# Optimization experiments

Hardware: AMD Instinct MI355X
Metric: run time of the kernel (lower is better)

Reference implementation:

```python
import jax, jax.numpy as jnp
import numpy as np
from jax import lax

DIM = 128
HEADS = 8
GROUPS = 8
DIM_HEAD = 64
DOWN = 4
OFF_SCALE = 4.0
KSIZE = 6
B, N, M = 2, 1024, 1024


def ln(x, g, b, eps=1e-5):
    m = x.mean(-1, keepdims=True)
    v = ((x - m) ** 2).mean(-1, keepdims=True)
    return (x - m) / jnp.sqrt(v + eps) * g + b


def grid_sample_1d(feats, grid):
    # feats: (Bg, C, Mk), grid: (Bg, Nd) normalized coords in [-1, 1]
    # bilinear, padding_mode='zeros', align_corners=False (torch semantics)
    Bg, C, Mk = feats.shape
    x = ((grid + 1.0) * Mk - 1.0) / 2.0
    x0 = jnp.floor(x)
    w1 = x - x0

    def gather(xi):
        valid = ((xi >= 0) & (xi <= Mk - 1)).astype(feats.dtype)
        idx = jnp.clip(xi, 0, Mk - 1).astype(jnp.int32)
        vals = jnp.take_along_axis(
            feats, jnp.broadcast_to(idx[:, None, :], (Bg, C, idx.shape[-1])), axis=2)
        return vals * valid[:, None, :]

    return gather(x0) * (1.0 - w1)[:, None, :] + gather(x0 + 1.0) * w1[:, None, :]


def deform_cross_attn(xq, xkv, qw, kw, vw, ow, ob, o1w, o1b, o2w,
                      c1w, c1b, c2w, c2b, c3w, c3b):
    # xq, xkv: (B, C, N) channel-first token streams
    Bb, C, Nq = xq.shape
    cg = C // GROUPS  # 16 channels per offset group
    q = jnp.einsum('bgcn,goc->bgon', xq.reshape(Bb, GROUPS, cg, Nq), qw)  # (B,g,64,N)
    gq = q.reshape(Bb * GROUPS, DIM_HEAD, Nq)
    pad = (KSIZE - DOWN) // 2
    off = lax.conv_general_dilated(gq, o1w[:, None, :], (DOWN,), [(pad, pad)],
                                   feature_group_count=DIM_HEAD,
                                   dimension_numbers=('NCH', 'OIH', 'NCH')) + o1b[None, :, None]
    off = jax.nn.gelu(off, approximate=False)
    off = jnp.tanh(jnp.einsum('bcn,c->bn', off, o2w)) * OFF_SCALE  # (B*g, Nd)
    Nd = off.shape[-1]
    vgrid = jnp.arange(Nd, dtype=off.dtype)[None] + off
    vgs = 2.0 * vgrid / max(Nd - 1, 1) - 1.0  # normalized sample positions
    xkv_g = xkv.reshape(Bb, GROUPS, cg, xkv.shape[-1]).reshape(Bb * GROUPS, cg, xkv.shape[-1])
    kv = grid_sample_1d(xkv_g, vgs).reshape(Bb, GROUPS, cg, Nd)
    k = jnp.einsum('bgcn,goc->bgon', kv, kw)
    v = jnp.einsum('bgcn,goc->bgon', kv, vw)
    sim = jnp.einsum('bhdi,bhdj->bhij', q * (DIM_HEAD ** -0.5), k)  # heads == groups
    seq = 2.0 * jnp.arange(Nq, dtype=vgs.dtype) / max(Nq - 1, 1) - 1.0
    rel = seq[None, :, None] - vgs[:, None, :]  # (B*g, N, Nd)
    bias = jnp.sign(rel) * jnp.log1p(jnp.abs(rel))
    h = jax.nn.relu(bias[..., None] * c1w[0] + c1b)  # CPB MLP, hidden=dim//4=32
    h = jax.nn.relu(h @ c2w + c2b)
    h = (h @ c3w + c3b)[..., 0]
    sim = sim + h.reshape(Bb, GROUPS, Nq, Nd)  # heads // offset_groups == 1
    attn = jax.nn.softmax(sim, axis=-1)
    out = jnp.einsum('bhij,bhdj->bhdi', attn, v).reshape(Bb, GROUPS * DIM_HEAD, Nq)
    out = jnp.einsum('bcn,oc->bon', out, ow) + ob[:, None]
    return out, attn


def mha(q_in, kv_in, w_in, b_in, w_out, b_out):
    # seq-first torch nn.MultiheadAttention, eval mode (no dropout)
    E = DIM; h = HEADS; dh = E // h
    q = q_in @ w_in[:E].T + b_in[:E]
    k = kv_in @ w_in[E:2 * E].T + b_in[E:2 * E]
    v = kv_in @ w_in[2 * E:].T + b_in[2 * E:]
    Lq, Bb, _ = q.shape
    Lk = k.shape[0]
    qh = q.reshape(Lq, Bb, h, dh).transpose(1, 2, 0, 3)
    kh = k.reshape(Lk, Bb, h, dh).transpose(1, 2, 0, 3)
    vh = v.reshape(Lk, Bb, h, dh).transpose(1, 2, 0, 3)
    attn = jax.nn.softmax(jnp.einsum('bhid,bhjd->bhij', qh, kh) * (dh ** -0.5), axis=-1)
    out = jnp.einsum('bhij,bhjd->bhid', attn, vh).transpose(2, 0, 1, 3).reshape(Lq, Bb, E)
    return out @ w_out.T + b_out


def transfusion(x1, x2, ng, nb, inw, inb, ow, ob, pw, pb):
    x = x1 + mha(ln(x1, ng, nb), ln(x2, ng, nb), inw, inb, ow, ob)
    x = ln(x.transpose(1, 0, 2), ng, nb)  # (B, N, E)
    return jnp.tanh(x.mean(1) @ pw.T + pb)[:, None, :]  # (B, 1, E)


def setup_inputs():
    key = jax.random.key(0)
    ks = iter(jax.random.split(key, 40))
    rn = lambda shape, s=0.05: jax.random.normal(next(ks), shape, dtype=jnp.float32) * s
    return {
        'x1_0': rn((B, N, DIM), 1.0),
        'x1_1': rn((B, N, DIM), 1.0),
        'x2': rn((B, M, DIM), 1.0),
        'norm_g': jnp.ones((DIM,), jnp.float32),
        'norm_b': jnp.zeros((DIM,), jnp.float32),
        'd_qw': rn((2, GROUPS, DIM_HEAD, DIM // GROUPS)),
        'd_kw': rn((2, GROUPS, DIM_HEAD, DIM // GROUPS)),
        'd_vw': rn((2, GROUPS, DIM_HEAD, DIM // GROUPS)),
        'd_ow': rn((2, DIM, GROUPS * DIM_HEAD)),
        'd_ob': jnp.zeros((2, DIM), jnp.float32),
        'd_off1w': rn((2, DIM_HEAD, KSIZE)),
        'd_off1b': jnp.zeros((2, DIM_HEAD), jnp.float32),
        'd_off2w': rn((2, DIM_HEAD)),
        'd_cpb_w1': rn((2, 1, 32)),
        'd_cpb_b1': jnp.zeros((2, 32), jnp.float32),
        'd_cpb_w2': rn((2, 32, 32)),
        'd_cpb_b2': jnp.zeros((2, 32), jnp.float32),
        'd_cpb_w3': rn((2, 32, 1)),
        'd_cpb_b3': jnp.zeros((2, 1), jnp.float32),
        'fus_w': rn((DIM, 2 * DIM)),
        'fus_b': jnp.zeros((DIM,), jnp.float32),
        'tf_ng': jnp.ones((2, DIM), jnp.float32),
        'tf_nb': jnp.zeros((2, DIM), jnp.float32),
        'tf_inw': rn((2, 3 * DIM, DIM)),
        'tf_inb': jnp.zeros((2, 3 * DIM), jnp.float32),
        'tf_ow': rn((2, DIM, DIM)),
        'tf_ob': jnp.zeros((2, DIM), jnp.float32),
        'tf_pw': rn((2, DIM, DIM)),
        'tf_pb': jnp.zeros((2, DIM), jnp.float32),
        'attn_dim': 128,
    }


def reference(x1_0, x1_1, x2, norm_g, norm_b, d_qw, d_kw, d_vw, d_ow, d_ob,
              d_off1w, d_off1b, d_off2w, d_cpb_w1, d_cpb_b1, d_cpb_w2, d_cpb_b2,
              d_cpb_w3, d_cpb_b3, fus_w, fus_b, tf_ng, tf_nb, tf_inw, tf_inb,
              tf_ow, tf_ob, tf_pw, tf_pb, attn_dim):
    nkv = ln(x2, norm_g, norm_b).transpose(0, 2, 1)
    xo1, a1 = deform_cross_attn(ln(x1_0, norm_g, norm_b).transpose(0, 2, 1), nkv,
                                d_qw[0], d_kw[0], d_vw[0], d_ow[0], d_ob[0],
                                d_off1w[0], d_off1b[0], d_off2w[0],
                                d_cpb_w1[0], d_cpb_b1[0], d_cpb_w2[0], d_cpb_b2[0],
                                d_cpb_w3[0], d_cpb_b3[0])
    xo2, a2 = deform_cross_attn(ln(x1_1, norm_g, norm_b).transpose(0, 2, 1), nkv,
                                d_qw[1], d_kw[1], d_vw[1], d_ow[1], d_ob[1],
                                d_off1w[1], d_off1b[1], d_off2w[1],
                                d_cpb_w1[1], d_cpb_b1[1], d_cpb_w2[1], d_cpb_b2[1],
                                d_cpb_w3[1], d_cpb_b3[1])
    xout1 = x1_0 + xo1.transpose(0, 2, 1)
    xout2 = x1_1 + xo2.transpose(0, 2, 1)
    x = jnp.concatenate([xout1, xout2], axis=-1) @ fus_w.T + fus_b
    query = ln(x, norm_g, norm_b).transpose(1, 0, 2)
    kv1 = ln(x1_0[:, :1, :], norm_g, norm_b).transpose(1, 0, 2)
    kv2 = ln(x1_1[:, :1, :], norm_g, norm_b).transpose(1, 0, 2)
    f1 = transfusion(query, kv1, tf_ng[0], tf_nb[0], tf_inw[0], tf_inb[0],
                     tf_ow[0], tf_ob[0], tf_pw[0], tf_pb[0])
    f2 = transfusion(query, kv2, tf_ng[1], tf_nb[1], tf_inw[1], tf_inb[1],
                     tf_ow[1], tf_ob[1], tf_pw[1], tf_pb[1])
    return (f1, f2, a1, a2)
```

## Files before the change

kernel.cpp:

```cpp
#include <hip/hip_runtime.h>
#include <hip/hip_bf16.h>


namespace {

constexpr int kN  = 1024;
constexpr int kC  = 128;
constexpr int kG  = 8;
constexpr int kDH = 64;
constexpr int kND = 256;

constexpr int   kNT    = 2048;
constexpr float kRLO   = -2.0625f;
constexpr float kRSPAN = 4.125f;

constexpr size_t W_LNKV = 0;
constexpr size_t W_LNQ1 = 262144;
constexpr size_t W_LNQ2 = 524288;
constexpr size_t W_Q    = 786432;
constexpr size_t W_K    = 1835008;
constexpr size_t W_VT   = 2097152;
constexpr size_t W_VGS  = 2359296;
constexpr size_t W_AO   = 2367488;
constexpr size_t W_TAB  = 5251072;
constexpr size_t W_MOUT = 5283844;
constexpr size_t W_PART = 5284356;
constexpr size_t W_OWB  = 5317124;
constexpr size_t W_FWB  = 5382660;

}

typedef __attribute__((ext_vector_type(8))) short short8;
typedef __attribute__((ext_vector_type(4))) float floatx4;

__device__ __forceinline__ float wave_sum(float v) {
#pragma unroll
  for (int o = 32; o > 0; o >>= 1) v += __shfl_xor(v, o, 64);
  return v;
}
__device__ __forceinline__ float bf_lo(unsigned int u) {
  return __uint_as_float(u << 16);
}
__device__ __forceinline__ float bf_hi(unsigned int u) {
  return __uint_as_float(u & 0xffff0000u);
}
__device__ __forceinline__ float cpb_lds(const float* __restrict__ tabL,
                                         float seq, float vg) {
  float rel = seq - vg;
  float ft = (rel - kRLO) * ((float)kNT / kRSPAN);
  ft = fminf(fmaxf(ft, 0.f), (float)kNT - 0.001f);
  int ix = (int)ft;
  float fw = ft - (float)ix;
  return tabL[ix] * (1.f - fw) + tabL[ix + 1] * fw;
}
__device__ __forceinline__ float dot128_v4(const float* __restrict__ wrow,
                                           const float* __restrict__ svec) {
  const float4* w4 = (const float4*)wrow;
  const float4* s4 = (const float4*)svec;
  float a0 = 0.f, a1 = 0.f, a2 = 0.f, a3 = 0.f;
#pragma unroll 8
  for (int c = 0; c < 32; ++c) {
    float4 wv = w4[c], sv = s4[c];
    a0 += wv.x * sv.x; a1 += wv.y * sv.y;
    a2 += wv.z * sv.z; a3 += wv.w * sv.w;
  }
  return (a0 + a1) + (a2 + a3);
}

__global__ void k_prep(const float* __restrict__ ow, const float* __restrict__ fw,
                       __hip_bfloat16* __restrict__ owb, __hip_bfloat16* __restrict__ fwb,
                       const float* __restrict__ x1_0, const float* __restrict__ x1_1,
                       const float* __restrict__ x2, float* __restrict__ lnq1,
                       float* __restrict__ lnq2, float* __restrict__ lnkv,
                       const float* __restrict__ ng, const float* __restrict__ nb,
                       const float* __restrict__ cw1, const float* __restrict__ cb1,
                       const float* __restrict__ cw2, const float* __restrict__ cb2,
                       const float* __restrict__ cw3, const float* __restrict__ cb3,
                       float* __restrict__ tab,
                       const float* __restrict__ tfng, const float* __restrict__ tfnb,
                       const float* __restrict__ inw, const float* __restrict__ inb,
                       const float* __restrict__ tow, const float* __restrict__ tob,
                       float* __restrict__ mout) {
  int bx = blockIdx.x;
  int t = threadIdx.x;
  if (bx < 640) {
    int id = bx * 256 + t;
    if (id < 131072) owb[id] = __float2bfloat16(ow[id]);
    else fwb[id - 131072] = __float2bfloat16(fw[id - 131072]);
  } else if (bx < 2176) {
    int w = t >> 6, lane = t & 63;
    int gr = (bx - 640) * 4 + w;
    int sel = gr >> 11, row = gr & 2047;
    const float* in = (sel == 0) ? x1_0 : (sel == 1) ? x1_1 : x2;
    float* out = (sel == 0) ? lnq1 : (sel == 1) ? lnq2 : lnkv;
    const float* xr = in + (size_t)row * kC;
    float xa = xr[lane], xb = xr[lane + 64];
    float m = wave_sum(xa + xb) * (1.f / kC);
    float da = xa - m, db = xb - m;
    float v = wave_sum(da * da + db * db) * (1.f / kC);
    float r = rsqrtf(v + 1e-5f);
    float* orow = out + (size_t)row * kC;
    orow[lane]      = da * r * ng[lane] + nb[lane];
    orow[lane + 64] = db * r * ng[lane + 64] + nb[lane + 64];
  } else if (bx < 2194) {
    int rel = bx - 2176;
    int idx = rel / 9, bb = rel - idx * 9;
    int tt = bb * 256 + t;
    if (tt <= kNT) {
      float rel_ = kRLO + (kRSPAN / (float)kNT) * (float)tt;
      float u = (rel_ >= 0.f ? 1.f : -1.f) * log1pf(fabsf(rel_));
      const float* W1 = cw1 + idx * 32; const float* B1 = cb1 + idx * 32;
      const float* W2 = cw2 + idx * 1024; const float* B2 = cb2 + idx * 32;
      const float* W3 = cw3 + idx * 32; const float* B3 = cb3 + idx;
      float h1[32];
#pragma unroll
      for (int m = 0; m < 32; ++m) h1[m] = fmaxf(0.f, u * W1[m] + B1[m]);
      float o = B3[0];
      for (int m = 0; m < 32; ++m) {
        float a = B2[m];
#pragma unroll
        for (int k = 0; k < 32; ++k) a += h1[k] * W2[k * 32 + m];
        o += fmaxf(a, 0.f) * W3[m];
      }
      tab[(size_t)idx * (kNT + 1) + tt] = o;
    }
  } else {
    int rel = bx - 2194;
    int i = rel >> 1, b = rel & 1;
    bool act = t < 128;
    __shared__ float red[2];
    __shared__ __align__(16) float s1[128];
    __shared__ __align__(16) float s2[128];
    const float* xs = (i ? x1_1 : x1_0) + (size_t)b * kN * kC;
    float x = act ? xs[t] : 0.f;
    float s = wave_sum(x);
    if (act && (t & 63) == 0) red[t >> 6] = s;
    __syncthreads();
    float m1 = (red[0] + red[1]) * (1.f / kC);
    __syncthreads();
    float d1 = x - m1;
    float ss = wave_sum(act ? d1 * d1 : 0.f);
    if (act && (t & 63) == 0) red[t >> 6] = ss;
    __syncthreads();
    float v1 = (red[0] + red[1]) * (1.f / kC);
    __syncthreads();
    float t0 = act ? d1 * rsqrtf(v1 + 1e-5f) * ng[t] + nb[t] : 0.f;
    s = wave_sum(t0);
    if (act && (t & 63) == 0) red[t >> 6] = s;
    __syncthreads();
    float m2 = (red[0] + red[1]) * (1.f / kC);
    __syncthreads();
    float d2 = t0 - m2;
    ss = wave_sum(act ? d2 * d2 : 0.f);
    if (act && (t & 63) == 0) red[t >> 6] = ss;
    __syncthreads();
    float v2 = (red[0] + red[1]) * (1.f / kC);
    if (act) s1[t] = d2 * rsqrtf(v2 + 1e-5f) * tfng[i * kC + t] + tfnb[i * kC + t];
    __syncthreads();
    if (act) {
      const float* wr = inw + (size_t)i * 384 * kC + (size_t)(256 + t) * kC;
      s2[t] = inb[i * 384 + 256 + t] + dot128_v4(wr, s1);
    }
    __syncthreads();
    if (act) {
      const float* wr2 = tow + (size_t)i * kC * kC + (size_t)t * kC;
      mout[rel * kC + t] = tob[i * kC + t] + dot128_v4(wr2, s2);
    }
  }
}

__global__ void k_qoff(const float* __restrict__ lnq1, const float* __restrict__ lnq2,
                       const float* __restrict__ qw, const float* __restrict__ o1w,
                       const float* __restrict__ o1b, const float* __restrict__ o2w,
                       __hip_bfloat16* __restrict__ qout, float* __restrict__ vgs) {
  int bx = blockIdx.x;
  if (bx < 512) {
    int bg = bx >> 4, r0 = (bx & 15) * 64;
    int str = bg >> 4, b = (bg >> 3) & 1, g = bg & 7;
    int rl = threadIdx.x & 63, dq = threadIdx.x >> 6;
    const float* lnq = str ? lnq2 : lnq1;
    const float* xr = lnq + ((size_t)(b * kN + r0 + rl)) * kC + g * 16;
    float4 x0 = *(const float4*)(xr + 0);
    float4 x1 = *(const float4*)(xr + 4);
    float4 x2 = *(const float4*)(xr + 8);
    float4 x3 = *(const float4*)(xr + 12);
    const float* wqb = qw + (size_t)str * 8192 + (size_t)g * 1024;
    __hip_bfloat16* qrow = qout + ((size_t)bg * 1024 + r0 + rl) * 64 + dq * 16;
#pragma unroll 4
    for (int dd = 0; dd < 16; ++dd) {
      int d = dq * 16 + dd;
      const float* wq = wqb + d * 16;
      float4 w0 = *(const float4*)(wq + 0);
      float4 w1 = *(const float4*)(wq + 4);
      float4 w2 = *(const float4*)(wq + 8);
      float4 w3 = *(const float4*)(wq + 12);
      float q = x0.x * w0.x + x0.y * w0.y + x0.z * w0.z + x0.w * w0.w
              + x1.x * w1.x + x1.y * w1.y + x1.z * w1.z + x1.w * w1.w
              + x2.x * w2.x + x2.y * w2.y + x2.z * w2.z + x2.w * w2.w
              + x3.x * w3.x + x3.y * w3.y + x3.z * w3.z + x3.w * w3.w;
      qrow[dd] = __float2bfloat16(q);
    }
  } else {
    int bxo = bx - 512;
    int w = threadIdx.x >> 6, lane = threadIdx.x & 63;
    int bg = bxo >> 6, j = ((bxo & 63) << 2) + w;
    int str = bg >> 4, b = (bg >> 3) & 1, g = bg & 7;
    const float* lnq = str ? lnq2 : lnq1;
    __shared__ float xr[4][96];
    int base = j * 4 - 1;
#pragma unroll
    for (int rep = 0; rep < 2; ++rep) {
      int idx = lane + rep * 64;
      if (idx < 96) {
        int r = idx >> 4, c = idx & 15, n = base + r;
        xr[w][idx] = (n >= 0 && n < kN)
                         ? lnq[((size_t)(b * kN + n)) * kC + g * 16 + c] : 0.f;
      }
    }
    const float* wq = qw + (size_t)str * 8192 + (size_t)(g * kDH + lane) * 16;
    float acc = o1b[str * 64 + lane];
#pragma unroll
    for (int k2 = 0; k2 < 6; ++k2) {
      float qv = 0.f;
#pragma unroll
      for (int c = 0; c < 16; ++c) qv += xr[w][k2 * 16 + c] * wq[c];
      acc += qv * o1w[str * 384 + lane * 6 + k2];
    }
    float ge = 0.5f * acc * (1.f + erff(acc * 0.70710678118654752440f));
    float s = wave_sum(ge * o2w[str * 64 + lane]);
    if (lane == 0)
      vgs[bg * kND + j] = 2.f * ((float)j + tanhf(s) * 4.0f) / 255.f - 1.f;
  }
}

__global__ void k_sample_kv(const float* __restrict__ lnkv, const float* __restrict__ vgs,
                            const float* __restrict__ kw, const float* __restrict__ vw,
                            __hip_bfloat16* __restrict__ kout,
                            __hip_bfloat16* __restrict__ vtout) {
  int w = threadIdx.x >> 6, lane = threadIdx.x & 63;
  int bg = blockIdx.x >> 6, j = ((blockIdx.x & 63) << 2) + w;
  int str = bg >> 4, b = (bg >> 3) & 1, g = bg & 7;
  __shared__ float sc[4][16];
  if (lane < 16) {
    float gr = vgs[bg * kND + j];
    float x = ((gr + 1.f) * 1024.f - 1.f) * 0.5f;
    float x0f = floorf(x);
    float w1 = x - x0f;
    int x0 = (int)x0f, x1 = x0 + 1;
    const float* src = lnkv + (size_t)b * kN * kC + g * 16 + lane;
    float v0 = (x0 >= 0 && x0 < 1024) ? src[(size_t)x0 * kC] : 0.f;
    float v1 = (x1 >= 0 && x1 < 1024) ? src[(size_t)x1 * kC] : 0.f;
    sc[w][lane] = v0 * (1.f - w1) + v1 * w1;
  }
  const float* kwr = kw + (size_t)str * 8192 + (size_t)(g * kDH + lane) * 16;
  const float* vwr = vw + (size_t)str * 8192 + (size_t)(g * kDH + lane) * 16;
  float ka = 0.f, va = 0.f;
#pragma unroll
  for (int c = 0; c < 16; ++c) { ka += sc[w][c] * kwr[c]; va += sc[w][c] * vwr[c]; }
  kout[((size_t)bg * 256 + j) * 64 + lane] = __float2bfloat16(ka);
  vtout[((size_t)bg * 64 + lane) * 256 + j] = __float2bfloat16(va);
}

__global__ void __launch_bounds__(256, 2)
k_attn(const __hip_bfloat16* __restrict__ q_g, const __hip_bfloat16* __restrict__ k_g,
       const __hip_bfloat16* __restrict__ vt_g, const float* __restrict__ vgs,
       const float* __restrict__ tab, float* __restrict__ aout,
       __hip_bfloat16* __restrict__ attout) {
  int bg = blockIdx.x >> 4, tile = blockIdx.x & 15;
  int str = bg >> 4;
  int i0 = tile * 64;
  int t = threadIdx.x;
  int w = t >> 6, l = t & 63;
  int lr = l & 15, lg = l >> 4;

  __shared__ __align__(16) __hip_bfloat16 Qs[64 * 72];
  __shared__ __align__(16) __hip_bfloat16 KVs[256 * 72];
  __shared__ __align__(16) __hip_bfloat16 Ps[64 * 264];

  const float* tabs = tab + str * (kNT + 1);

  {
    const __hip_bfloat16* qflat = q_g + ((size_t)bg * 1024 + i0) * 64;
#pragma unroll
    for (int i2 = 0; i2 < 2; ++i2) {
      int e = i2 * 2048 + t * 8;
      int r = e >> 6, c = e & 63;
      *(float4*)&Qs[r * 72 + c] = *(const float4*)(qflat + e);
    }
    const __hip_bfloat16* kflat = k_g + (size_t)bg * 256 * 64;
#pragma unroll
    for (int i2 = 0; i2 < 8; ++i2) {
      int e = i2 * 2048 + t * 8;
      int r = e >> 6, c = e & 63;
      *(float4*)&KVs[r * 72 + c] = *(const float4*)(kflat + e);
    }
  }
  __syncthreads();

  short8 a0 = *(const short8*)&Qs[(w * 16 + lr) * 72 + lg * 8];
  short8 a1 = *(const short8*)&Qs[(w * 16 + lr) * 72 + 32 + lg * 8];
  __syncthreads();
  float* tabL = (float*)Qs;
  for (int e = t; e <= kNT; e += 256) tabL[e] = tabs[e];

  floatx4 acc[16];
#pragma unroll
  for (int f = 0; f < 16; ++f) acc[f] = {0.f, 0.f, 0.f, 0.f};
#pragma unroll
  for (int ct = 0; ct < 16; ++ct) {
    short8 b0 = *(const short8*)&KVs[(ct * 16 + lr) * 72 + lg * 8];
    short8 b1 = *(const short8*)&KVs[(ct * 16 + lr) * 72 + 32 + lg * 8];
    acc[ct] = __builtin_amdgcn_mfma_f32_16x16x32_bf16(a0, b0, acc[ct], 0, 0, 0);
    acc[ct] = __builtin_amdgcn_mfma_f32_16x16x32_bf16(a1, b1, acc[ct], 0, 0, 0);
  }
  __syncthreads();

  float4 vr0, vr1, vr2, vr3, vr4, vr5, vr6, vr7;
  {
    const __hip_bfloat16* vflat = vt_g + (size_t)bg * 64 * 256;
    vr0 = *(const float4*)(vflat + 0 * 2048 + t * 8);
    vr1 = *(const float4*)(vflat + 1 * 2048 + t * 8);
    vr2 = *(const float4*)(vflat + 2 * 2048 + t * 8);
    vr3 = *(const float4*)(vflat + 3 * 2048 + t * 8);
    vr4 = *(const float4*)(vflat + 4 * 2048 + t * 8);
    vr5 = *(const float4*)(vflat + 5 * 2048 + t * 8);
    vr6 = *(const float4*)(vflat + 6 * 2048 + t * 8);
    vr7 = *(const float4*)(vflat + 7 * 2048 + t * 8);
  }

  float vgl[16];
#pragma unroll
  for (int f = 0; f < 16; ++f) vgl[f] = vgs[bg * 256 + f * 16 + lr];
#pragma unroll
  for (int reg = 0; reg < 4; ++reg) {
    int row = w * 16 + lg * 4 + reg;
    int i = i0 + row;
    float seq = 2.f * (float)i / 1023.f - 1.f;
    float sv[16];
#pragma unroll
    for (int f = 0; f < 16; ++f)
      sv[f] = acc[f][reg] * 0.125f + cpb_lds(tabL, seq, vgl[f]);
    float m = sv[0];
#pragma unroll
    for (int f = 1; f < 16; ++f) m = fmaxf(m, sv[f]);
    m = fmaxf(m, __shfl_xor(m, 1, 64));
    m = fmaxf(m, __shfl_xor(m, 2, 64));
    m = fmaxf(m, __shfl_xor(m, 4, 64));
    m = fmaxf(m, __shfl_xor(m, 8, 64));
    float ev[16], sum = 0.f;
#pragma unroll
    for (int f = 0; f < 16; ++f) { ev[f] = __expf(sv[f] - m); sum += ev[f]; }
    sum += __shfl_xor(sum, 1, 64);
    sum += __shfl_xor(sum, 2, 64);
    sum += __shfl_xor(sum, 4, 64);
    sum += __shfl_xor(sum, 8, 64);
    float inv = 1.f / sum;
#pragma unroll
    for (int f = 0; f < 16; ++f)
      Ps[row * 264 + f * 16 + lr] = __float2bfloat16(ev[f] * inv);
  }

  {
    int e0 = t * 8;
#pragma unroll
    for (int i2 = 0; i2 < 8; ++i2) {
      int e = i2 * 2048 + e0;
      int r = e >> 8, c = e & 255;
      float4 v = (i2 == 0) ? vr0 : (i2 == 1) ? vr1 : (i2 == 2) ? vr2 :
                 (i2 == 3) ? vr3 : (i2 == 4) ? vr4 : (i2 == 5) ? vr5 :
                 (i2 == 6) ? vr6 : vr7;
      *(float4*)&KVs[r * 264 + c] = v;
    }
  }
  __syncthreads();

  {
    float* aoutb = aout + (size_t)str * 4194304 + (size_t)(bg & 15) * 262144 +
                   (size_t)i0 * 256;
#pragma unroll
    for (int it = 0; it < 16; ++it) {
      int e = it * 1024 + t * 4;
      int row = e >> 8, col = e & 255;
      unsigned int p2a = *(const unsigned int*)&Ps[row * 264 + col];
      unsigned int p2b = *(const unsigned int*)&Ps[row * 264 + col + 2];
      float4 o = {bf_lo(p2a), bf_hi(p2a), bf_lo(p2b), bf_hi(p2b)};
      *(float4*)&aoutb[(size_t)row * 256 + col] = o;
    }
  }

  floatx4 oacc[4];
#pragma unroll
  for (int dt = 0; dt < 4; ++dt) oacc[dt] = {0.f, 0.f, 0.f, 0.f};
#pragma unroll
  for (int ks = 0; ks < 8; ++ks) {
    short8 pa = *(const short8*)&Ps[(w * 16 + lr) * 264 + ks * 32 + lg * 8];
#pragma unroll
    for (int dt = 0; dt < 4; ++dt) {
      short8 b = *(const short8*)&KVs[(dt * 16 + lr) * 264 + ks * 32 + lg * 8];
      oacc[dt] = __builtin_amdgcn_mfma_f32_16x16x32_bf16(pa, b, oacc[dt], 0, 0, 0);
    }
  }

  {
    __hip_bfloat16* Ob = Qs;
#pragma unroll
    for (int dt = 0; dt < 4; ++dt)
#pragma unroll
      for (int reg = 0; reg < 4; ++reg)
        Ob[(w * 16 + lg * 4 + reg) * 72 + dt * 16 + lr] =
            __float2bfloat16(oacc[dt][reg]);
    int r = t >> 2, c0 = (t & 3) * 16;
    float4 o0 = *(const float4*)&Ob[r * 72 + c0];
    float4 o1 = *(const float4*)&Ob[r * 72 + c0 + 8];
    int b = (bg >> 3) & 1, g = bg & 7;
    __hip_bfloat16* ab = attout + ((size_t)(str * 2 + b) * 1024 + i0 + r) * 512 +
                         (size_t)g * 64 + c0;
    *(float4*)ab = o0;
    *(float4*)(ab + 8) = o1;
  }
}

__global__ void __launch_bounds__(256, 2)
k_oproj_fuse(const __hip_bfloat16* __restrict__ aog, const __hip_bfloat16* __restrict__ owb,
             const float* __restrict__ ob,
             const float* __restrict__ x1_0, const float* __restrict__ x1_1,
             const __hip_bfloat16* __restrict__ fwb, const float* __restrict__ fb,
             const float* __restrict__ ng, const float* __restrict__ nb,
             const float* __restrict__ tfng, const float* __restrict__ tfnb,
             const float* __restrict__ mout, float* __restrict__ partial) {
  int tok0 = blockIdx.x * 16;
  int t = threadIdx.x;
  int w = t >> 6, l = t & 63;
  int lr = l & 15, lg = l >> 4;
  int nt0 = w * 2;

  __shared__ __align__(16) unsigned char smem[16 * 280 * 2];
  __shared__ float red[4][128];
  __hip_bfloat16* xos = (__hip_bfloat16*)smem;
  float* fs = (float*)smem;

  for (int s = 0; s < 2; ++s) {
    const __hip_bfloat16* arow = aog + ((size_t)(s * 2048 + tok0 + lr)) * 512 + lg * 8;
    const __hip_bfloat16* wb0 = owb + (size_t)s * 65536 + (size_t)((nt0 + 0) * 16 + lr) * 512 + lg * 8;
    const __hip_bfloat16* wb1 = owb + (size_t)s * 65536 + (size_t)((nt0 + 1) * 16 + lr) * 512 + lg * 8;
    floatx4 acc0 = {0.f, 0.f, 0.f, 0.f}, acc1 = {0.f, 0.f, 0.f, 0.f};
#pragma unroll
    for (int ks = 0; ks < 16; ++ks) {
      short8 a  = *(const short8*)(arow + ks * 32);
      short8 b0 = *(const short8*)(wb0 + ks * 32);
      short8 b1 = *(const short8*)(wb1 + ks * 32);
      acc0 = __builtin_amdgcn_mfma_f32_16x16x32_bf16(a, b0, acc0, 0, 0, 0);
      acc1 = __builtin_amdgcn_mfma_f32_16x16x32_bf16(a, b1, acc1, 0, 0, 0);
    }
    const float* x1 = s ? x1_1 : x1_0;
    float bias0 = ob[s * 128 + nt0 * 16 + lr];
    float bias1 = ob[s * 128 + (nt0 + 1) * 16 + lr];
#pragma unroll
    for (int reg = 0; reg < 4; ++reg) {
      int row = lg * 4 + reg;
      size_t xi = (size_t)(tok0 + row) * 128;
      xos[row * 280 + s * 128 + nt0 * 16 + lr] =
          __float2bfloat16(acc0[reg] + x1[xi + nt0 * 16 + lr] + bias0);
      xos[row * 280 + s * 128 + (nt0 + 1) * 16 + lr] =
          __float2bfloat16(acc1[reg] + x1[xi + (nt0 + 1) * 16 + lr] + bias1);
    }
  }
  __syncthreads();

  floatx4 f0 = {0.f, 0.f, 0.f, 0.f}, f1 = {0.f, 0.f, 0.f, 0.f};
  const __hip_bfloat16* fb0 = fwb + (size_t)((nt0 + 0) * 16 + lr) * 256 + lg * 8;
  const __hip_bfloat16* fb1 = fwb + (size_t)((nt0 + 1) * 16 + lr) * 256 + lg * 8;
#pragma unroll
  for (int ks = 0; ks < 8; ++ks) {
    short8 a  = *(const short8*)&xos[lr * 280 + ks * 32 + lg * 8];
    short8 b0 = *(const short8*)(fb0 + ks * 32);
    short8 b1 = *(const short8*)(fb1 + ks * 32);
    f0 = __builtin_amdgcn_mfma_f32_16x16x32_bf16(a, b0, f0, 0, 0, 0);
    f1 = __builtin_amdgcn_mfma_f32_16x16x32_bf16(a, b1, f1, 0, 0, 0);
  }
  __syncthreads();

  {
    float fbias0 = fb[nt0 * 16 + lr], fbias1 = fb[(nt0 + 1) * 16 + lr];
#pragma unroll
    for (int reg = 0; reg < 4; ++reg) {
      int row = lg * 4 + reg;
      fs[row * 132 + w * 32 + lr]      = f0[reg] + fbias0;
      fs[row * 132 + w * 32 + 16 + lr] = f1[reg] + fbias1;
    }
  }
  __syncthreads();

  int b = tok0 >> 10, chunk = (tok0 & 1023) >> 4;
  float g1a = ng[l], b1a = nb[l], g1b = ng[l + 64], b1b = nb[l + 64];
  float mo0a = mout[b * 128 + l], mo0b = mout[b * 128 + l + 64];
  float mo1a = mout[(2 + b) * 128 + l], mo1b = mout[(2 + b) * 128 + l + 64];
  float g20a = tfng[l], b20a = tfnb[l], g20b = tfng[l + 64], b20b = tfnb[l + 64];
  float g21a = tfng[128 + l], b21a = tfnb[128 + l];
  float g21b = tfng[192 + l], b21b = tfnb[192 + l];
  float acc0a = 0.f, acc0b = 0.f, acc1a = 0.f, acc1b = 0.f;
#pragma unroll
  for (int it = 0; it < 4; ++it) {
    int tok = it * 4 + w;
    float xa = fs[tok * 132 + l], xb = fs[tok * 132 + l + 64];
    float m1 = wave_sum(xa + xb) * (1.f / kC);
    float da = xa - m1, db = xb - m1;
    float v1 = wave_sum(da * da + db * db) * (1.f / kC);
    float r1 = rsqrtf(v1 + 1e-5f);
    float ba = da * r1 * g1a + b1a, bb = db * r1 * g1b + b1b;
    {
      float za = ba + mo0a, zb = bb + mo0b;
      float m2 = wave_sum(za + zb) * (1.f / kC);
      float ea = za - m2, eb = zb - m2;
      float v2 = wave_sum(ea * ea + eb * eb) * (1.f / kC);
      float r2 = rsqrtf(v2 + 1e-5f);
      acc0a += ea * r2 * g20a + b20a;
      acc0b += eb * r2 * g20b + b20b;
    }
    {
      float za = ba + mo1a, zb = bb + mo1b;
      float m2 = wave_sum(za + zb) * (1.f / kC);
      float ea = za - m2, eb = zb - m2;
      float v2 = wave_sum(ea * ea + eb * eb) * (1.f / kC);
      float r2 = rsqrtf(v2 + 1e-5f);
      acc1a += ea * r2 * g21a + b21a;
      acc1b += eb * r2 * g21b + b21b;
    }
  }
  red[w][l] = acc0a; red[w][l + 64] = acc0b;
  __syncthreads();
  if (w == 0) {
    float* pr = partial + ((size_t)(b)*64 + chunk) * kC;
    pr[l]      = red[0][l] + red[1][l] + red[2][l] + red[3][l];
    pr[l + 64] = red[0][l + 64] + red[1][l + 64] + red[2][l + 64] + red[3][l + 64];
  }
  __syncthreads();
  red[w][l] = acc1a; red[w][l + 64] = acc1b;
  __syncthreads();
  if (w == 0) {
    float* pr = partial + ((size_t)(2 + b) * 64 + chunk) * kC;
    pr[l]      = red[0][l] + red[1][l] + red[2][l] + red[3][l];
    pr[l + 64] = red[0][l + 64] + red[1][l + 64] + red[2][l + 64] + red[3][l + 64];
  }
}

__global__ void k_final(const float* __restrict__ partial, const float* __restrict__ pw,
                        const float* __restrict__ pb, float* __restrict__ out) {
  int ib = blockIdx.x;
  int i = ib >> 1, t = threadIdx.x;
  int c = t & 127, half = t >> 7;
  float a = 0.f;
  for (int ch = half * 32; ch < half * 32 + 32; ++ch)
    a += partial[((size_t)ib * 64 + ch) * kC + c];
  __shared__ __align__(16) float s[256];
  s[half * 128 + c] = a;
  __syncthreads();
  if (t < 128) s[t] = (s[t] + s[128 + t]) * (1.f / (float)kN);
  __syncthreads();
  if (t < 128) {
    const float* wr = pw + (size_t)i * kC * kC + (size_t)t * kC;
    out[ib * 128 + t] = tanhf(pb[i * kC + t] + dot128_v4(wr, s));
  }
}

extern "C" void kernel_launch(void* const* d_in, const int* in_sizes, int n_in,
                              void* d_out, int out_size, void* d_ws, size_t ws_size,
                              hipStream_t stream) {
  const float* x1_0   = (const float*)d_in[0];
  const float* x1_1   = (const float*)d_in[1];
  const float* x2     = (const float*)d_in[2];
  const float* norm_g = (const float*)d_in[3];
  const float* norm_b = (const float*)d_in[4];
  const float* d_qw   = (const float*)d_in[5];
  const float* d_kw   = (const float*)d_in[6];
  const float* d_vw   = (const float*)d_in[7];
  const float* d_ow   = (const float*)d_in[8];
  const float* d_ob   = (const float*)d_in[9];
  const float* d_o1w  = (const float*)d_in[10];
  const float* d_o1b  = (const float*)d_in[11];
  const float* d_o2w  = (const float*)d_in[12];
  const float* c_w1   = (const float*)d_in[13];
  const float* c_b1   = (const float*)d_in[14];
  const float* c_w2   = (const float*)d_in[15];
  const float* c_b2   = (const float*)d_in[16];
  const float* c_w3   = (const float*)d_in[17];
  const float* c_b3   = (const float*)d_in[18];
  const float* fus_w  = (const float*)d_in[19];
  const float* fus_b  = (const float*)d_in[20];
  const float* tf_ng  = (const float*)d_in[21];
  const float* tf_nb  = (const float*)d_in[22];
  const float* tf_inw = (const float*)d_in[23];
  const float* tf_inb = (const float*)d_in[24];
  const float* tf_ow  = (const float*)d_in[25];
  const float* tf_ob  = (const float*)d_in[26];
  const float* tf_pw  = (const float*)d_in[27];
  const float* tf_pb  = (const float*)d_in[28];

  float* ws = (float*)d_ws;
  float* out = (float*)d_out;
  float* lnkv = ws + W_LNKV;
  float* lnq1 = ws + W_LNQ1; float* lnq2 = ws + W_LNQ2;
  __hip_bfloat16* qb  = (__hip_bfloat16*)(ws + W_Q);
  __hip_bfloat16* kb  = (__hip_bfloat16*)(ws + W_K);
  __hip_bfloat16* vtb = (__hip_bfloat16*)(ws + W_VT);
  float* vgsw = ws + W_VGS;
  __hip_bfloat16* aob = (__hip_bfloat16*)(ws + W_AO);
  float* tab = ws + W_TAB;
  float* moutp = ws + W_MOUT; float* partp = ws + W_PART;
  __hip_bfloat16* owb = (__hip_bfloat16*)(ws + W_OWB);
  __hip_bfloat16* fwb = (__hip_bfloat16*)(ws + W_FWB);

  float* aoutb = out + 512;

  k_prep<<<2198, 256, 0, stream>>>(d_ow, fus_w, owb, fwb,
                                   x1_0, x1_1, x2, lnq1, lnq2, lnkv, norm_g, norm_b,
                                   c_w1, c_b1, c_w2, c_b2, c_w3, c_b3, tab,
                                   tf_ng, tf_nb, tf_inw, tf_inb, tf_ow, tf_ob, moutp);
  k_qoff<<<2560, 256, 0, stream>>>(lnq1, lnq2, d_qw, d_o1w, d_o1b, d_o2w, qb, vgsw);
  k_sample_kv<<<2048, 256, 0, stream>>>(lnkv, vgsw, d_kw, d_vw, kb, vtb);
  k_attn<<<512, 256, 0, stream>>>(qb, kb, vtb, vgsw, tab, aoutb, aob);
  k_oproj_fuse<<<128, 256, 0, stream>>>(aob, owb, d_ob, x1_0, x1_1, fwb, fus_b,
                                        norm_g, norm_b, tf_ng, tf_nb, moutp, partp);
  k_final<<<4, 256, 0, stream>>>(partp, tf_pw, tf_pb, out);

  (void)in_sizes; (void)n_in; (void)out_size; (void)ws_size;
}
```

Before: 85.04 us.

## Split fused out-projection kernel into two higher-parallelism kernels

The fused out-projection plus fusion/LayerNorm kernel ran on only 128 blocks. It is now two kernels: a 512-block out-projection that writes residual-added bf16 rows to a workspace buffer, and a 256-block fusion-and-mean kernel that handles 8 tokens per block. The partial-sum layout and the final reduction are widened to 128 chunks to match. This should fill the GPU better, at the cost of an extra launch, a global round trip for the intermediate, and MFMA rows wasted in the 8-token fusion tiles.

```diff
diff --git a/kernel.cpp b/kernel.cpp
--- a/kernel.cpp
+++ b/kernel.cpp
@@ -25,8 +25,9 @@
 constexpr size_t W_TAB  = 5251072;
 constexpr size_t W_MOUT = 5283844;
 constexpr size_t W_PART = 5284356;
-constexpr size_t W_OWB  = 5317124;
-constexpr size_t W_FWB  = 5382660;
+constexpr size_t W_OWB  = 5349892;
+constexpr size_t W_FWB  = 5415428;
+constexpr size_t W_XOB  = 5431812;
 
 }
 
@@ -421,77 +422,79 @@
 }
 
 __global__ void __launch_bounds__(256, 2)
-k_oproj_fuse(const __hip_bfloat16* __restrict__ aog, const __hip_bfloat16* __restrict__ owb,
-             const float* __restrict__ ob,
-             const float* __restrict__ x1_0, const float* __restrict__ x1_1,
-             const __hip_bfloat16* __restrict__ fwb, const float* __restrict__ fb,
+k_oproj(const __hip_bfloat16* __restrict__ aog, const __hip_bfloat16* __restrict__ owb,
+        const float* __restrict__ ob, const float* __restrict__ x1_0,
+        const float* __restrict__ x1_1, __hip_bfloat16* __restrict__ xob) {
+  int bid = blockIdx.x;
+  int nq = bid & 1, tg = (bid >> 1) & 127, s = bid >> 8;
+  int t = threadIdx.x;
+  int w = t >> 6, l = t & 63;
+  int lr = l & 15, lg = l >> 4;
+  int nt = nq * 4 + w;
+
+  const __hip_bfloat16* arow = aog + ((size_t)(s * 2048 + tg * 16 + lr)) * 512 + lg * 8;
+  const __hip_bfloat16* wb = owb + (size_t)s * 65536 + (size_t)(nt * 16 + lr) * 512 + lg * 8;
+  floatx4 acc = {0.f, 0.f, 0.f, 0.f};
+#pragma unroll
+  for (int ks = 0; ks < 16; ++ks) {
+    short8 a = *(const short8*)(arow + ks * 32);
+    short8 b = *(const short8*)(wb + ks * 32);
+    acc = __builtin_amdgcn_mfma_f32_16x16x32_bf16(a, b, acc, 0, 0, 0);
+  }
+  const float* x1 = s ? x1_1 : x1_0;
+  float bias = ob[s * 128 + nt * 16 + lr];
+#pragma unroll
+  for (int reg = 0; reg < 4; ++reg) {
+    int row = lg * 4 + reg;
+    int tok = tg * 16 + row;
+    xob[((size_t)s * 2064 + tok) * 128 + nt * 16 + lr] =
+        __float2bfloat16(acc[reg] + x1[(size_t)tok * 128 + nt * 16 + lr] + bias);
+  }
+}
+
+__global__ void __launch_bounds__(256, 2)
+k_fuse_meanz(const __hip_bfloat16* __restrict__ xob, const __hip_bfloat16* __restrict__ fwb,
+             const float* __restrict__ fb,
              const float* __restrict__ ng, const float* __restrict__ nb,
              const float* __restrict__ tfng, const float* __restrict__ tfnb,
              const float* __restrict__ mout, float* __restrict__ partial) {
-  int tok0 = blockIdx.x * 16;
+  int tg = blockIdx.x;
   int t = threadIdx.x;
   int w = t >> 6, l = t & 63;
   int lr = l & 15, lg = l >> 4;
   int nt0 = w * 2;
 
-  __shared__ __align__(16) unsigned char smem[16 * 280 * 2];
+  __shared__ __align__(16) float fs[8 * 132];
   __shared__ float red[4][128];
-  __hip_bfloat16* xos = (__hip_bfloat16*)smem;
-  float* fs = (float*)smem;
-
-  for (int s = 0; s < 2; ++s) {
-    const __hip_bfloat16* arow = aog + ((size_t)(s * 2048 + tok0 + lr)) * 512 + lg * 8;
-    const __hip_bfloat16* wb0 = owb + (size_t)s * 65536 + (size_t)((nt0 + 0) * 16 + lr) * 512 + lg * 8;
-    const __hip_bfloat16* wb1 = owb + (size_t)s * 65536 + (size_t)((nt0 + 1) * 16 + lr) * 512 + lg * 8;
-    floatx4 acc0 = {0.f, 0.f, 0.f, 0.f}, acc1 = {0.f, 0.f, 0.f, 0.f};
-#pragma unroll
-    for (int ks = 0; ks < 16; ++ks) {
-      short8 a  = *(const short8*)(arow + ks * 32);
-      short8 b0 = *(const short8*)(wb0 + ks * 32);
-      short8 b1 = *(const short8*)(wb1 + ks * 32);
-      acc0 = __builtin_amdgcn_mfma_f32_16x16x32_bf16(a, b0, acc0, 0, 0, 0);
-      acc1 = __builtin_amdgcn_mfma_f32_16x16x32_bf16(a, b1, acc1, 0, 0, 0);
-    }
-    const float* x1 = s ? x1_1 : x1_0;
-    float bias0 = ob[s * 128 + nt0 * 16 + lr];
-    float bias1 = ob[s * 128 + (nt0 + 1) * 16 + lr];
-#pragma unroll
-    for (int reg = 0; reg < 4; ++reg) {
-      int row = lg * 4 + reg;
-      size_t xi = (size_t)(tok0 + row) * 128;
-      xos[row * 280 + s * 128 + nt0 * 16 + lr] =
-          __float2bfloat16(acc0[reg] + x1[xi + nt0 * 16 + lr] + bias0);
-      xos[row * 280 + s * 128 + (nt0 + 1) * 16 + lr] =
-          __float2bfloat16(acc1[reg] + x1[xi + (nt0 + 1) * 16 + lr] + bias1);
-    }
-  }
-  __syncthreads();
 
   floatx4 f0 = {0.f, 0.f, 0.f, 0.f}, f1 = {0.f, 0.f, 0.f, 0.f};
   const __hip_bfloat16* fb0 = fwb + (size_t)((nt0 + 0) * 16 + lr) * 256 + lg * 8;
   const __hip_bfloat16* fb1 = fwb + (size_t)((nt0 + 1) * 16 + lr) * 256 + lg * 8;
 #pragma unroll
   for (int ks = 0; ks < 8; ++ks) {
-    short8 a  = *(const short8*)&xos[lr * 280 + ks * 32 + lg * 8];
+    int sk = ks >> 2;
+    int koff = (ks & 3) * 32 + lg * 8;
+    short8 a = *(const short8*)(xob + ((size_t)sk * 2064 + tg * 8 + lr) * 128 + koff);
     short8 b0 = *(const short8*)(fb0 + ks * 32);
     short8 b1 = *(const short8*)(fb1 + ks * 32);
     f0 = __builtin_amdgcn_mfma_f32_16x16x32_bf16(a, b0, f0, 0, 0, 0);
     f1 = __builtin_amdgcn_mfma_f32_16x16x32_bf16(a, b1, f1, 0, 0, 0);
   }
-  __syncthreads();
-
   {
     float fbias0 = fb[nt0 * 16 + lr], fbias1 = fb[(nt0 + 1) * 16 + lr];
 #pragma unroll
     for (int reg = 0; reg < 4; ++reg) {
       int row = lg * 4 + reg;
-      fs[row * 132 + w * 32 + lr]      = f0[reg] + fbias0;
-      fs[row * 132 + w * 32 + 16 + lr] = f1[reg] + fbias1;
-    }
-  }
-  __syncthreads();
-
-  int b = tok0 >> 10, chunk = (tok0 & 1023) >> 4;
+      if (row < 8) {
+        fs[row * 132 + nt0 * 16 + lr]       = f0[reg] + fbias0;
+        fs[row * 132 + (nt0 + 1) * 16 + lr] = f1[reg] + fbias1;
+      }
+    }
+  }
+  __syncthreads();
+
+  int b = tg >> 7;
+  int chunk = tg & 127;
   float g1a = ng[l], b1a = nb[l], g1b = ng[l + 64], b1b = nb[l + 64];
   float mo0a = mout[b * 128 + l], mo0b = mout[b * 128 + l + 64];
   float mo1a = mout[(2 + b) * 128 + l], mo1b = mout[(2 + b) * 128 + l + 64];
@@ -500,7 +503,7 @@
   float g21b = tfng[192 + l], b21b = tfnb[192 + l];
   float acc0a = 0.f, acc0b = 0.f, acc1a = 0.f, acc1b = 0.f;
 #pragma unroll
-  for (int it = 0; it < 4; ++it) {
+  for (int it = 0; it < 2; ++it) {
     int tok = it * 4 + w;
     float xa = fs[tok * 132 + l], xb = fs[tok * 132 + l + 64];
     float m1 = wave_sum(xa + xb) * (1.f / kC);
@@ -530,7 +533,7 @@
   red[w][l] = acc0a; red[w][l + 64] = acc0b;
   __syncthreads();
   if (w == 0) {
-    float* pr = partial + ((size_t)(b)*64 + chunk) * kC;
+    float* pr = partial + ((size_t)(b)*128 + chunk) * kC;
     pr[l]      = red[0][l] + red[1][l] + red[2][l] + red[3][l];
     pr[l + 64] = red[0][l + 64] + red[1][l + 64] + red[2][l + 64] + red[3][l + 64];
   }
@@ -538,7 +541,7 @@
   red[w][l] = acc1a; red[w][l + 64] = acc1b;
   __syncthreads();
   if (w == 0) {
-    float* pr = partial + ((size_t)(2 + b) * 64 + chunk) * kC;
+    float* pr = partial + ((size_t)(2 + b) * 128 + chunk) * kC;
     pr[l]      = red[0][l] + red[1][l] + red[2][l] + red[3][l];
     pr[l + 64] = red[0][l + 64] + red[1][l + 64] + red[2][l + 64] + red[3][l + 64];
   }
@@ -550,8 +553,8 @@
   int i = ib >> 1, t = threadIdx.x;
   int c = t & 127, half = t >> 7;
   float a = 0.f;
-  for (int ch = half * 32; ch < half * 32 + 32; ++ch)
-    a += partial[((size_t)ib * 64 + ch) * kC + c];
+  for (int ch = half * 64; ch < half * 64 + 64; ++ch)
+    a += partial[((size_t)ib * 128 + ch) * kC + c];
   __shared__ __align__(16) float s[256];
   s[half * 128 + c] = a;
   __syncthreads();
@@ -609,6 +612,7 @@
   float* moutp = ws + W_MOUT; float* partp = ws + W_PART;
   __hip_bfloat16* owb = (__hip_bfloat16*)(ws + W_OWB);
   __hip_bfloat16* fwb = (__hip_bfloat16*)(ws + W_FWB);
+  __hip_bfloat16* xob = (__hip_bfloat16*)(ws + W_XOB);
 
   float* aoutb = out + 512;
 
@@ -619,8 +623,9 @@
   k_qoff<<<2560, 256, 0, stream>>>(lnq1, lnq2, d_qw, d_o1w, d_o1b, d_o2w, qb, vgsw);
   k_sample_kv<<<2048, 256, 0, stream>>>(lnkv, vgsw, d_kw, d_vw, kb, vtb);
   k_attn<<<512, 256, 0, stream>>>(qb, kb, vtb, vgsw, tab, aoutb, aob);
-  k_oproj_fuse<<<128, 256, 0, stream>>>(aob, owb, d_ob, x1_0, x1_1, fwb, fus_b,
-                                        norm_g, norm_b, tf_ng, tf_nb, moutp, partp);
+  k_oproj<<<512, 256, 0, stream>>>(aob, owb, d_ob, x1_0, x1_1, xob);
+  k_fuse_meanz<<<256, 256, 0, stream>>>(xob, fwb, fus_b, norm_g, norm_b,
+                                        tf_ng, tf_nb, moutp, partp);
   k_final<<<4, 256, 0, stream>>>(partp, tf_pw, tf_pb, out);
 
   (void)in_sizes; (void)n_in; (void)out_size; (void)ws_size;
```

Measured after the change: 96.12 us. +13.0%, slower.
